# Kernel optimization log

Hardware: AMD Instinct MI355X
Metric: run time of the kernel (lower is better)

Reference implementation:

```python
import jax, jax.numpy as jnp
import numpy as np

N, E, IN, HID, H, L, G = 20000, 320000, 128, 64, 4, 3, 128

def setup_inputs() -> dict:
    key = jax.random.key(0)
    ks = jax.random.split(key, 14)
    x = jax.random.normal(ks[0], (N, IN), dtype=jnp.float32)
    edge_index = jax.random.randint(ks[1], (2, E), 0, N, dtype=jnp.int64)
    batch = jnp.sort(jax.random.randint(ks[2], (N,), 0, G, dtype=jnp.int64))
    s_in = 1.0 / np.sqrt(IN)
    s_h = 1.0 / np.sqrt(HID)
    lin_W = jax.random.normal(ks[3], (IN, HID), jnp.float32) * s_in
    lin_b = jax.random.normal(ks[4], (HID,), jnp.float32) * 0.02
    Wq = jax.random.normal(ks[5], (L, HID, H * HID), jnp.float32) * s_h
    bq = jax.random.normal(ks[6], (L, H * HID), jnp.float32) * 0.02
    Wk = jax.random.normal(ks[7], (L, HID, H * HID), jnp.float32) * s_h
    bk = jax.random.normal(ks[8], (L, H * HID), jnp.float32) * 0.02
    Wv = jax.random.normal(ks[9], (L, HID, H * HID), jnp.float32) * s_h
    bv = jax.random.normal(ks[10], (L, H * HID), jnp.float32) * 0.02
    Ws = jax.random.normal(ks[11], (L, HID, HID), jnp.float32) * s_h
    bs = jax.random.normal(ks[12], (L, HID), jnp.float32) * 0.02
    return {"x": x, "edge_index": edge_index, "batch": batch,
            "lin_W": lin_W, "lin_b": lin_b, "Wq": Wq, "bq": bq,
            "Wk": Wk, "bk": bk, "Wv": Wv, "bv": bv, "Ws": Ws, "bs": bs}

def _transformer_conv(h, src, dst, Wq, bq, Wk, bk, Wv, bv, Ws, bs):
    # PyG TransformerConv(hid, hid, heads=H, concat=False), beta=False, root_weight=True
    n = h.shape[0]
    C = HID  # per-head dim
    q = (h @ Wq + bq).reshape(n, H, C)
    k = (h @ Wk + bk).reshape(n, H, C)
    v = (h @ Wv + bv).reshape(n, H, C)
    # per-edge attention logits: q_i . k_j / sqrt(C), i=dst (target), j=src
    alpha = jnp.einsum('ehc,ehc->eh', q[dst], k[src]) * (1.0 / np.sqrt(C))  # [E,H]
    # segment softmax over edges grouped by target node
    amax = jax.ops.segment_max(alpha, dst, num_segments=n)  # [N,H]
    amax = jnp.where(jnp.isfinite(amax), amax, 0.0)
    ex = jnp.exp(alpha - amax[dst])
    denom = jax.ops.segment_sum(ex, dst, num_segments=n)
    a = ex / jnp.maximum(denom[dst], 1e-16)  # [E,H]
    msg = a[:, :, None] * v[src]  # [E,H,C]
    agg = jax.ops.segment_sum(msg.reshape(-1, H * C), dst, num_segments=n)
    out = agg.reshape(n, H, C).mean(axis=1)  # concat=False -> head mean
    return out + h @ Ws + bs  # root/skip connection

def reference(x, edge_index, batch, lin_W, lin_b, Wq, bq, Wk, bk, Wv, bv, Ws, bs):
    src, dst = edge_index[0], edge_index[1]
    h = x @ lin_W + lin_b  # [N, HID]; dropout inactive in eval
    for l in range(L):
        h = jax.nn.relu(_transformer_conv(h, src, dst, Wq[l], bq[l], Wk[l], bk[l],
                                          Wv[l], bv[l], Ws[l], bs[l]))
    # global_add_pool: sum node features per graph
    return jax.ops.segment_sum(h, batch, num_segments=G)  # [G, HID]
```

## Files before the change

### kernel.cpp

```cpp
#include <hip/hip_runtime.h>
#include <math.h>

#define N_NODES 20000
#define N_EDGES 320000
#define DIM_IN 128
#define HID 64
#define HEADS 4
#define LAYERS 3
#define GRAPHS 128
#define QSS 320

typedef unsigned short ushort;
typedef ushort ushort8 __attribute__((ext_vector_type(8)));
typedef short short8 __attribute__((ext_vector_type(8)));
typedef float f32x4 __attribute__((ext_vector_type(4)));

__device__ __forceinline__ float bf2f(ushort u) {
    return __uint_as_float(((unsigned int)u) << 16);
}
__device__ __forceinline__ ushort f2bf(float f) {
    unsigned int b = __float_as_uint(f);
    return (ushort)((b + 0x7FFFu + ((b >> 16) & 1u)) >> 16);
}


__global__ void hist_kernel(const int* __restrict__ dst, int* __restrict__ counts, int n) {
    int e = blockIdx.x * 256 + threadIdx.x;
    if (e < n) atomicAdd(&counts[dst[e]], 1);
}

__global__ __launch_bounds__(256) void blocksum_kernel(const int* __restrict__ counts,
                                                       int* __restrict__ bsum, int n) {
    int i = blockIdx.x * 256 + threadIdx.x;
    int v = (i < n) ? counts[i] : 0;
    int lane = threadIdx.x & 63, wave = threadIdx.x >> 6;
#pragma unroll
    for (int off = 32; off >= 1; off >>= 1) v += __shfl_xor(v, off);
    __shared__ int ws[4];
    if (lane == 0) ws[wave] = v;
    __syncthreads();
    if (threadIdx.x == 0) bsum[blockIdx.x] = ws[0] + ws[1] + ws[2] + ws[3];
}

__global__ __launch_bounds__(128) void scanb_kernel(const int* __restrict__ bsum,
                                                    int* __restrict__ bexcl, int nb) {
    int tid = threadIdx.x;
    int v = (tid < nb) ? bsum[tid] : 0;
    int lane = tid & 63, wave = tid >> 6;
    int s = v;
#pragma unroll
    for (int off = 1; off < 64; off <<= 1) {
        int t = __shfl_up(s, off);
        if (lane >= off) s += t;
    }
    __shared__ int w0sum;
    if (tid == 63) w0sum = s;
    __syncthreads();
    int excl = s - v + (wave ? w0sum : 0);
    if (tid < nb) bexcl[tid] = excl;
}

__global__ __launch_bounds__(256) void expand_kernel(const int* __restrict__ counts,
                                                     const int* __restrict__ bexcl,
                                                     int* __restrict__ offs,
                                                     int* __restrict__ cursor, int n) {
    int i = blockIdx.x * 256 + threadIdx.x;
    int v = (i < n) ? counts[i] : 0;
    int lane = threadIdx.x & 63, wave = threadIdx.x >> 6;
    int s = v;
#pragma unroll
    for (int off = 1; off < 64; off <<= 1) {
        int t = __shfl_up(s, off);
        if (lane >= off) s += t;
    }
    __shared__ int wsum[4];
    if (lane == 63) wsum[wave] = s;
    __syncthreads();
    int add = bexcl[blockIdx.x];
    for (int w = 0; w < wave; ++w) add += wsum[w];
    int excl = add + s - v;
    if (i < n) { offs[i] = excl; cursor[i] = excl; }
    if (i == 0) offs[n] = N_EDGES;
}

__global__ void scatter_kernel(const int* __restrict__ src, const int* __restrict__ dst,
                               int* __restrict__ cursor, int* __restrict__ csr, int n) {
    int e = blockIdx.x * 256 + threadIdx.x;
    if (e < n) {
        int d = dst[e];
        int pos = atomicAdd(&cursor[d], 1);
        csr[pos] = src[e];
    }
}


__global__ __launch_bounds__(256) void lin_kernel(const float* __restrict__ x,
                                                  const float* __restrict__ W,
                                                  const float* __restrict__ b,
                                                  float* __restrict__ h0) {
    __shared__ float xt[32][DIM_IN];
    int tx = threadIdx.x;
    int row0 = blockIdx.x * 32;
    for (int idx = tx; idx < 32 * DIM_IN; idx += 256) {
        int r = idx / DIM_IN, c = idx % DIM_IN;
        xt[r][c] = x[(size_t)(row0 + r) * DIM_IN + c];
    }
    __syncthreads();
    int col = tx & 63;
    int sub = tx >> 6;
    float acc[8];
#pragma unroll
    for (int r = 0; r < 8; ++r) acc[r] = 0.f;
    for (int k = 0; k < DIM_IN; k += 4) {
        float w0 = W[k * HID + col];
        float w1 = W[(k + 1) * HID + col];
        float w2 = W[(k + 2) * HID + col];
        float w3 = W[(k + 3) * HID + col];
#pragma unroll
        for (int r = 0; r < 8; ++r) {
            const float4 hv = *(const float4*)&xt[r * 4 + sub][k];
            acc[r] += hv.x * w0 + hv.y * w1 + hv.z * w2 + hv.w * w3;
        }
    }
    float bias = b[col];
#pragma unroll
    for (int r = 0; r < 8; ++r) {
        int row = row0 + r * 4 + sub;
        h0[(size_t)row * HID + col] = acc[r] + bias;
    }
}


__global__ __launch_bounds__(256) void wcvt_kernel(const float* __restrict__ Wq, const float* __restrict__ bq,
                                                   const float* __restrict__ Wk, const float* __restrict__ bk,
                                                   const float* __restrict__ Wv, const float* __restrict__ bv,
                                                   const float* __restrict__ Ws, const float* __restrict__ bs,
                                                   ushort* __restrict__ Wt, float* __restrict__ bias_cat) {
    int idx = blockIdx.x * 256 + threadIdx.x;
    if (idx < 832 * 64) {
        int j = idx >> 6, k = idx & 63;
        float w;
        if (j < 256)      w = Wq[(size_t)k * 256 + j];
        else if (j < 512) w = Wk[(size_t)k * 256 + (j - 256)];
        else if (j < 768) w = Wv[(size_t)k * 256 + (j - 512)];
        else              w = Ws[(size_t)k * 64 + (j - 768)];
        Wt[idx] = f2bf(w);
    }
    if (idx < 832) {
        float b;
        if (idx < 256)      b = bq[idx];
        else if (idx < 512) b = bk[idx - 256];
        else if (idx < 768) b = bv[idx - 512];
        else                b = bs[idx - 768];
        bias_cat[idx] = b;
    }
}


__global__ __launch_bounds__(512) void proj_kernel(const float* __restrict__ h,
                                                   const ushort* __restrict__ Wt,
                                                   const float* __restrict__ bias_cat,
                                                   float* __restrict__ qs,
                                                   ushort* __restrict__ kvpack) {
    int tid = threadIdx.x;
    int w = tid >> 6, l = tid & 63;
    int r0 = blockIdx.x * 32 + (w & 1) * 16;
    int c0 = (w >> 1) * 208;
    int row = r0 + (l & 15);
    int koff = (l >> 4) * 8;

    short8 a[2];
#pragma unroll
    for (int m = 0; m < 2; ++m) {
        const float* hp = h + (size_t)row * HID + m * 32 + koff;
        float4 f0 = *(const float4*)hp;
        float4 f1 = *(const float4*)(hp + 4);
        ushort8 u;
        u[0] = f2bf(f0.x); u[1] = f2bf(f0.y); u[2] = f2bf(f0.z); u[3] = f2bf(f0.w);
        u[4] = f2bf(f1.x); u[5] = f2bf(f1.y); u[6] = f2bf(f1.z); u[7] = f2bf(f1.w);
        a[m] = __builtin_bit_cast(short8, u);
    }

    f32x4 acc[13];
#pragma unroll
    for (int t = 0; t < 13; ++t) acc[t] = (f32x4){0.f, 0.f, 0.f, 0.f};

    const ushort* wb = Wt + ((size_t)(c0 + (l & 15))) * HID + koff;
#pragma unroll
    for (int t = 0; t < 13; ++t) {
        short8 b0 = *(const short8*)(wb + (size_t)t * 16 * HID);
        short8 b1 = *(const short8*)(wb + (size_t)t * 16 * HID + 32);
        acc[t] = __builtin_amdgcn_mfma_f32_16x16x32_bf16(a[0], b0, acc[t], 0, 0, 0);
        acc[t] = __builtin_amdgcn_mfma_f32_16x16x32_bf16(a[1], b1, acc[t], 0, 0, 0);
    }

    int colbase = c0 + (l & 15);
    int rbase = r0 + ((l >> 4) << 2);
#pragma unroll
    for (int t = 0; t < 13; ++t) {
        int j = colbase + t * 16;
        float bias = bias_cat[j];
        if (j < 256) {
#pragma unroll
            for (int i = 0; i < 4; ++i)
                qs[(size_t)(rbase + i) * QSS + j] = acc[t][i] + bias;
        } else if (j < 768) {
            int ck = j - 256;
            int isv = ck >> 8;
            int ch = ck & 255;
            int hh2 = ch >> 6, c = ch & 63;
            int pos = (hh2 * 16 + (c >> 2)) * 8 + isv * 4 + (c & 3);
#pragma unroll
            for (int i = 0; i < 4; ++i)
                kvpack[(size_t)(rbase + i) * 512 + pos] = f2bf(acc[t][i] + bias);
        } else {
#pragma unroll
            for (int i = 0; i < 4; ++i)
                qs[(size_t)(rbase + i) * QSS + 256 + (j - 768)] = acc[t][i] + bias;
        }
    }
}


__global__ __launch_bounds__(256) void edge_kernel(const float* __restrict__ qs,
                                                   const ushort8* __restrict__ kvp,
                                                   const int* __restrict__ offs,
                                                   const int* __restrict__ csr,
                                                   float* __restrict__ hout) {
    int wave = threadIdx.x >> 6;
    int lane = threadIdx.x & 63;
    int node = blockIdx.x * 4 + wave;
    if (node >= N_NODES) return;
    int hh = lane >> 4;
    int cb = (lane & 15) * 4;

    const float* nb = qs + (size_t)node * QSS;
    float4 q = *(const float4*)(nb + hh * 64 + cb);

    float m = -INFINITY, l = 0.f;
    float4 acc = make_float4(0.f, 0.f, 0.f, 0.f);

    int e0 = offs[node], e1 = offs[node + 1];
    int cnt = e1 - e0;

    ushort8 cur = (ushort8)(0);
    ushort8 nxt = (ushort8)(0);
    if (cnt > 0) cur = kvp[(size_t)csr[e0] * 64 + lane];
    if (cnt > 1) nxt = kvp[(size_t)csr[e0 + 1] * 64 + lane];

    for (int i = 0; i < cnt; ++i) {
        ushort8 u = cur;
        cur = nxt;
        if (i + 2 < cnt) nxt = kvp[(size_t)csr[e0 + i + 2] * 64 + lane];

        float p = q.x * bf2f(u[0]) + q.y * bf2f(u[1]) + q.z * bf2f(u[2]) + q.w * bf2f(u[3]);
        p += __shfl_xor(p, 1);
        p += __shfl_xor(p, 2);
        p += __shfl_xor(p, 4);
        p += __shfl_xor(p, 8);
        float alpha = p * 0.125f;
        float nm = fmaxf(m, alpha);
        float sc = __expf(m - nm);
        float pe = __expf(alpha - nm);
        l = l * sc + pe;
        acc.x = acc.x * sc + pe * bf2f(u[4]);
        acc.y = acc.y * sc + pe * bf2f(u[5]);
        acc.z = acc.z * sc + pe * bf2f(u[6]);
        acc.w = acc.w * sc + pe * bf2f(u[7]);
        m = nm;
    }

    float inv = (l > 0.f) ? (1.f / l) : 0.f;
    float4 r;
    r.x = acc.x * inv;
    r.y = acc.y * inv;
    r.z = acc.z * inv;
    r.w = acc.w * inv;
    r.x += __shfl_xor(r.x, 16); r.x += __shfl_xor(r.x, 32);
    r.y += __shfl_xor(r.y, 16); r.y += __shfl_xor(r.y, 32);
    r.z += __shfl_xor(r.z, 16); r.z += __shfl_xor(r.z, 32);
    r.w += __shfl_xor(r.w, 16); r.w += __shfl_xor(r.w, 32);

    if (hh == 0) {
        float4 s = *(const float4*)(nb + 256 + cb);
        float4 o;
        o.x = fmaxf(r.x * 0.25f + s.x, 0.f);
        o.y = fmaxf(r.y * 0.25f + s.y, 0.f);
        o.z = fmaxf(r.z * 0.25f + s.z, 0.f);
        o.w = fmaxf(r.w * 0.25f + s.w, 0.f);
        *(float4*)(hout + (size_t)node * HID + cb) = o;
    }
}


__global__ __launch_bounds__(256) void pool_kernel(const float* __restrict__ h,
                                                   const int* __restrict__ batch,
                                                   float* __restrict__ out) {
    int g = blockIdx.x;
    int lo = 0, hi = N_NODES;
    while (lo < hi) { int mid = (lo + hi) >> 1; if (batch[mid] < g) lo = mid + 1; else hi = mid; }
    int start = lo;
    hi = N_NODES;
    while (lo < hi) { int mid = (lo + hi) >> 1; if (batch[mid] < g + 1) lo = mid + 1; else hi = mid; }
    int end = lo;
    int c = threadIdx.x & 63;
    int sub = threadIdx.x >> 6;
    float acc = 0.f;
    for (int i = start + sub; i < end; i += 4) acc += h[(size_t)i * HID + c];
    __shared__ float lds[4][64];
    lds[sub][c] = acc;
    __syncthreads();
    if (sub == 0) out[g * HID + c] = lds[0][c] + lds[1][c] + lds[2][c] + lds[3][c];
}


extern "C" void kernel_launch(void* const* d_in, const int* in_sizes, int n_in,
                              void* d_out, int out_size, void* d_ws, size_t ws_size,
                              hipStream_t stream) {
    const float* x    = (const float*)d_in[0];
    const int*   edge = (const int*)d_in[1];
    const int*   batch= (const int*)d_in[2];
    const float* linW = (const float*)d_in[3];
    const float* linb = (const float*)d_in[4];
    const float* Wq   = (const float*)d_in[5];
    const float* bq   = (const float*)d_in[6];
    const float* Wk   = (const float*)d_in[7];
    const float* bk   = (const float*)d_in[8];
    const float* Wv   = (const float*)d_in[9];
    const float* bv   = (const float*)d_in[10];
    const float* Ws   = (const float*)d_in[11];
    const float* bs   = (const float*)d_in[12];
    float* out = (float*)d_out;

    const int* src = edge;
    const int* dst = edge + N_EDGES;

    float* h0  = (float*)d_ws;
    float* h1  = h0 + (size_t)N_NODES * HID;
    float* qs  = h1 + (size_t)N_NODES * HID;
    ushort* kvpack = (ushort*)(qs + (size_t)N_NODES * QSS);
    int* counts = (int*)(kvpack + (size_t)N_NODES * 512);
    int* offs   = counts + N_NODES;
    int* cursor = offs + N_NODES + 1;
    int* csr    = cursor + N_NODES;
    int* bsum   = csr + N_EDGES;
    int* bexcl  = bsum + 128;
    ushort* Wt  = (ushort*)(bexcl + 128);
    float* bias_cat = (float*)(Wt + 832 * 64);

    const int NB = (N_NODES + 255) / 256;

    hipMemsetAsync(counts, 0, N_NODES * sizeof(int), stream);
    hist_kernel<<<(N_EDGES + 255) / 256, 256, 0, stream>>>(dst, counts, N_EDGES);
    blocksum_kernel<<<NB, 256, 0, stream>>>(counts, bsum, N_NODES);
    scanb_kernel<<<1, 128, 0, stream>>>(bsum, bexcl, NB);
    expand_kernel<<<NB, 256, 0, stream>>>(counts, bexcl, offs, cursor, N_NODES);
    scatter_kernel<<<(N_EDGES + 255) / 256, 256, 0, stream>>>(src, dst, cursor, csr, N_EDGES);

    lin_kernel<<<N_NODES / 32, 256, 0, stream>>>(x, linW, linb, h0);

    float* hc = h0;
    float* hn = h1;
    for (int l = 0; l < LAYERS; ++l) {
        wcvt_kernel<<<(832 * 64 + 255) / 256, 256, 0, stream>>>(
            Wq + (size_t)l * HID * 256, bq + (size_t)l * 256,
            Wk + (size_t)l * HID * 256, bk + (size_t)l * 256,
            Wv + (size_t)l * HID * 256, bv + (size_t)l * 256,
            Ws + (size_t)l * HID * 64,  bs + (size_t)l * 64,
            Wt, bias_cat);
        proj_kernel<<<N_NODES / 32, 512, 0, stream>>>(hc, Wt, bias_cat, qs, kvpack);
        edge_kernel<<<N_NODES / 4, 256, 0, stream>>>(qs, (const ushort8*)kvpack, offs, csr, hn);
        float* t = hc; hc = hn; hn = t;
    }

    pool_kernel<<<GRAPHS, 256, 0, stream>>>(hc, batch, out);
}
```

Before: 404.3 us.

## Batch weight conversion, MFMA input linear, and 8-deep edge prefetch with lazy rescale

Merges the three per-layer weight conversion launches, plus a bf16 transpose of the input linear weight, into one kernel. The K/V interleave permutation moves from proj_kernel's store into the weight layout, so stores become contiguous. The input linear layer switches from scalar FP32 to bf16 MFMA. The edge kernel now prefetches 8 neighbor rows at a time and rescales the online softmax only when some lane's max increases. Together these cut launches and hide gather latency, at the cost of more registers and bf16 rounding of the input x.

```diff
diff --git a/kernel.cpp b/kernel.cpp
--- a/kernel.cpp
+++ b/kernel.cpp
@@ -94,65 +94,111 @@
 }
 
 
+__global__ __launch_bounds__(256) void wcvt_all_kernel(
+        const float* __restrict__ Wq, const float* __restrict__ bq,
+        const float* __restrict__ Wk, const float* __restrict__ bk,
+        const float* __restrict__ Wv, const float* __restrict__ bv,
+        const float* __restrict__ Ws, const float* __restrict__ bs,
+        const float* __restrict__ linW,
+        ushort* __restrict__ Wt3, float* __restrict__ bias3,
+        ushort* __restrict__ Wlt) {
+    const int PER = 832 * 64;
+    int idx = blockIdx.x * 256 + threadIdx.x;
+    if (idx < 3 * PER) {
+        int l = idx / PER;
+        int r = idx - l * PER;
+        int j = r >> 6, k = r & 63;
+        const float* Wq_l = Wq + (size_t)l * HID * 256;
+        const float* Wk_l = Wk + (size_t)l * HID * 256;
+        const float* Wv_l = Wv + (size_t)l * HID * 256;
+        const float* Ws_l = Ws + (size_t)l * HID * 64;
+        float w;
+        if (j < 256) {
+            w = Wq_l[(size_t)k * 256 + j];
+        } else if (j < 768) {
+            int pout = j - 256;
+            int isv = (pout >> 2) & 1;
+            int low2 = pout & 3;
+            int g = pout >> 3;
+            int srccol = (g >> 4) * 64 + (g & 15) * 4 + low2;
+            w = isv ? Wv_l[(size_t)k * 256 + srccol] : Wk_l[(size_t)k * 256 + srccol];
+        } else {
+            w = Ws_l[(size_t)k * 64 + (j - 768)];
+        }
+        Wt3[idx] = f2bf(w);
+    } else {
+        int idx2 = idx - 3 * PER;
+        if (idx2 < 64 * DIM_IN) {
+            int col = idx2 >> 7, k = idx2 & 127;
+            Wlt[idx2] = f2bf(linW[(size_t)k * HID + col]);
+        }
+    }
+    if (idx < 3 * 832) {
+        int l = idx / 832, j = idx - l * 832;
+        float b;
+        if (j < 256) {
+            b = bq[l * 256 + j];
+        } else if (j < 768) {
+            int pout = j - 256;
+            int isv = (pout >> 2) & 1;
+            int low2 = pout & 3;
+            int g = pout >> 3;
+            int srccol = (g >> 4) * 64 + (g & 15) * 4 + low2;
+            b = isv ? bv[l * 256 + srccol] : bk[l * 256 + srccol];
+        } else {
+            b = bs[l * 64 + (j - 768)];
+        }
+        bias3[idx] = b;
+    }
+}
+
+
 __global__ __launch_bounds__(256) void lin_kernel(const float* __restrict__ x,
-                                                  const float* __restrict__ W,
-                                                  const float* __restrict__ b,
+                                                  const ushort* __restrict__ Wlt,
+                                                  const float* __restrict__ lb,
                                                   float* __restrict__ h0) {
-    __shared__ float xt[32][DIM_IN];
-    int tx = threadIdx.x;
-    int row0 = blockIdx.x * 32;
-    for (int idx = tx; idx < 32 * DIM_IN; idx += 256) {
-        int r = idx / DIM_IN, c = idx % DIM_IN;
-        xt[r][c] = x[(size_t)(row0 + r) * DIM_IN + c];
-    }
-    __syncthreads();
-    int col = tx & 63;
-    int sub = tx >> 6;
-    float acc[8];
-#pragma unroll
-    for (int r = 0; r < 8; ++r) acc[r] = 0.f;
-    for (int k = 0; k < DIM_IN; k += 4) {
-        float w0 = W[k * HID + col];
-        float w1 = W[(k + 1) * HID + col];
-        float w2 = W[(k + 2) * HID + col];
-        float w3 = W[(k + 3) * HID + col];
-#pragma unroll
-        for (int r = 0; r < 8; ++r) {
-            const float4 hv = *(const float4*)&xt[r * 4 + sub][k];
-            acc[r] += hv.x * w0 + hv.y * w1 + hv.z * w2 + hv.w * w3;
-        }
-    }
-    float bias = b[col];
-#pragma unroll
-    for (int r = 0; r < 8; ++r) {
-        int row = row0 + r * 4 + sub;
-        h0[(size_t)row * HID + col] = acc[r] + bias;
-    }
-}
-
-
-__global__ __launch_bounds__(256) void wcvt_kernel(const float* __restrict__ Wq, const float* __restrict__ bq,
-                                                   const float* __restrict__ Wk, const float* __restrict__ bk,
-                                                   const float* __restrict__ Wv, const float* __restrict__ bv,
-                                                   const float* __restrict__ Ws, const float* __restrict__ bs,
-                                                   ushort* __restrict__ Wt, float* __restrict__ bias_cat) {
-    int idx = blockIdx.x * 256 + threadIdx.x;
-    if (idx < 832 * 64) {
-        int j = idx >> 6, k = idx & 63;
-        float w;
-        if (j < 256)      w = Wq[(size_t)k * 256 + j];
-        else if (j < 512) w = Wk[(size_t)k * 256 + (j - 256)];
-        else if (j < 768) w = Wv[(size_t)k * 256 + (j - 512)];
-        else              w = Ws[(size_t)k * 64 + (j - 768)];
-        Wt[idx] = f2bf(w);
-    }
-    if (idx < 832) {
-        float b;
-        if (idx < 256)      b = bq[idx];
-        else if (idx < 512) b = bk[idx - 256];
-        else if (idx < 768) b = bv[idx - 512];
-        else                b = bs[idx - 768];
-        bias_cat[idx] = b;
+    int tid = threadIdx.x;
+    int w = tid >> 6, l = tid & 63;
+    int r0 = blockIdx.x * 64 + w * 16;
+    int row = r0 + (l & 15);
+    int rowc = (row < N_NODES) ? row : (N_NODES - 1);
+
+    short8 a[4];
+#pragma unroll
+    for (int kc = 0; kc < 4; ++kc) {
+        const float* xp = x + (size_t)rowc * DIM_IN + kc * 32 + (l >> 4) * 8;
+        float4 f0 = *(const float4*)xp;
+        float4 f1 = *(const float4*)(xp + 4);
+        ushort8 u;
+        u[0] = f2bf(f0.x); u[1] = f2bf(f0.y); u[2] = f2bf(f0.z); u[3] = f2bf(f0.w);
+        u[4] = f2bf(f1.x); u[5] = f2bf(f1.y); u[6] = f2bf(f1.z); u[7] = f2bf(f1.w);
+        a[kc] = __builtin_bit_cast(short8, u);
+    }
+
+    f32x4 acc[4];
+#pragma unroll
+    for (int t = 0; t < 4; ++t) acc[t] = (f32x4){0.f, 0.f, 0.f, 0.f};
+
+    const ushort* wb = Wlt + (size_t)(l & 15) * DIM_IN + (l >> 4) * 8;
+#pragma unroll
+    for (int t = 0; t < 4; ++t) {
+#pragma unroll
+        for (int kc = 0; kc < 4; ++kc) {
+            short8 b = *(const short8*)(wb + (size_t)t * 16 * DIM_IN + kc * 32);
+            acc[t] = __builtin_amdgcn_mfma_f32_16x16x32_bf16(a[kc], b, acc[t], 0, 0, 0);
+        }
+    }
+
+    int rbase = r0 + ((l >> 4) << 2);
+#pragma unroll
+    for (int t = 0; t < 4; ++t) {
+        int col = t * 16 + (l & 15);
+        float bias = lb[col];
+#pragma unroll
+        for (int i = 0; i < 4; ++i) {
+            int rr = rbase + i;
+            if (rr < N_NODES) h0[(size_t)rr * HID + col] = acc[t][i] + bias;
+        }
     }
 }
 
@@ -205,14 +251,10 @@
             for (int i = 0; i < 4; ++i)
                 qs[(size_t)(rbase + i) * QSS + j] = acc[t][i] + bias;
         } else if (j < 768) {
-            int ck = j - 256;
-            int isv = ck >> 8;
-            int ch = ck & 255;
-            int hh2 = ch >> 6, c = ch & 63;
-            int pos = (hh2 * 16 + (c >> 2)) * 8 + isv * 4 + (c & 3);
+            int pout = j - 256;
 #pragma unroll
             for (int i = 0; i < 4; ++i)
-                kvpack[(size_t)(rbase + i) * 512 + pos] = f2bf(acc[t][i] + bias);
+                kvpack[(size_t)(rbase + i) * 512 + pout] = f2bf(acc[t][i] + bias);
         } else {
 #pragma unroll
             for (int i = 0; i < 4; ++i)
@@ -221,6 +263,29 @@
     }
 }
 
+
+#define LD1(DST, EI) { int ee = (EI) < e1 ? (EI) : (e1 - 1); DST = kvp[(size_t)csr[ee] * 64 + lane]; }
+
+#define PROC(U, EI) do { \
+    float p = q.x * bf2f(U[0]) + q.y * bf2f(U[1]) + q.z * bf2f(U[2]) + q.w * bf2f(U[3]); \
+    p += __shfl_xor(p, 1); \
+    p += __shfl_xor(p, 2); \
+    p += __shfl_xor(p, 4); \
+    p += __shfl_xor(p, 8); \
+    float alpha = ((EI) < e1) ? p * 0.125f : -INFINITY; \
+    if (__any(alpha > m)) { \
+        float nm = fmaxf(m, alpha); \
+        float sc = __expf(m - nm); \
+        l *= sc; acc.x *= sc; acc.y *= sc; acc.z *= sc; acc.w *= sc; \
+        m = nm; \
+    } \
+    float pe = __expf(alpha - m); \
+    l += pe; \
+    acc.x += pe * bf2f(U[4]); \
+    acc.y += pe * bf2f(U[5]); \
+    acc.z += pe * bf2f(U[6]); \
+    acc.w += pe * bf2f(U[7]); \
+} while (0)
 
 __global__ __launch_bounds__(256) void edge_kernel(const float* __restrict__ qs,
                                                    const ushort8* __restrict__ kvp,
@@ -243,31 +308,24 @@
     int e0 = offs[node], e1 = offs[node + 1];
     int cnt = e1 - e0;
 
-    ushort8 cur = (ushort8)(0);
-    ushort8 nxt = (ushort8)(0);
-    if (cnt > 0) cur = kvp[(size_t)csr[e0] * 64 + lane];
-    if (cnt > 1) nxt = kvp[(size_t)csr[e0 + 1] * 64 + lane];
-
-    for (int i = 0; i < cnt; ++i) {
-        ushort8 u = cur;
-        cur = nxt;
-        if (i + 2 < cnt) nxt = kvp[(size_t)csr[e0 + i + 2] * 64 + lane];
-
-        float p = q.x * bf2f(u[0]) + q.y * bf2f(u[1]) + q.z * bf2f(u[2]) + q.w * bf2f(u[3]);
-        p += __shfl_xor(p, 1);
-        p += __shfl_xor(p, 2);
-        p += __shfl_xor(p, 4);
-        p += __shfl_xor(p, 8);
-        float alpha = p * 0.125f;
-        float nm = fmaxf(m, alpha);
-        float sc = __expf(m - nm);
-        float pe = __expf(alpha - nm);
-        l = l * sc + pe;
-        acc.x = acc.x * sc + pe * bf2f(u[4]);
-        acc.y = acc.y * sc + pe * bf2f(u[5]);
-        acc.z = acc.z * sc + pe * bf2f(u[6]);
-        acc.w = acc.w * sc + pe * bf2f(u[7]);
-        m = nm;
+    if (cnt > 0) {
+        ushort8 A0, A1, A2, A3, A4, A5, A6, A7;
+        LD1(A0, e0 + 0); LD1(A1, e0 + 1); LD1(A2, e0 + 2); LD1(A3, e0 + 3);
+        LD1(A4, e0 + 4); LD1(A5, e0 + 5); LD1(A6, e0 + 6); LD1(A7, e0 + 7);
+        for (int base = e0; base < e1; base += 8) {
+            ushort8 B0, B1, B2, B3, B4, B5, B6, B7;
+            bool more = (base + 8) < e1;
+            if (more) {
+                LD1(B0, base + 8);  LD1(B1, base + 9);  LD1(B2, base + 10); LD1(B3, base + 11);
+                LD1(B4, base + 12); LD1(B5, base + 13); LD1(B6, base + 14); LD1(B7, base + 15);
+            }
+            PROC(A0, base + 0); PROC(A1, base + 1); PROC(A2, base + 2); PROC(A3, base + 3);
+            PROC(A4, base + 4); PROC(A5, base + 5); PROC(A6, base + 6); PROC(A7, base + 7);
+            if (more) {
+                A0 = B0; A1 = B1; A2 = B2; A3 = B3;
+                A4 = B4; A5 = B5; A6 = B6; A7 = B7;
+            }
+        }
     }
 
     float inv = (l > 0.f) ? (1.f / l) : 0.f;
@@ -345,8 +403,9 @@
     int* csr    = cursor + N_NODES;
     int* bsum   = csr + N_EDGES;
     int* bexcl  = bsum + 128;
-    ushort* Wt  = (ushort*)(bexcl + 128);
-    float* bias_cat = (float*)(Wt + 832 * 64);
+    ushort* Wt3 = (ushort*)(bexcl + 128);
+    float* bias3 = (float*)(Wt3 + 3 * 832 * 64);
+    ushort* Wlt = (ushort*)(bias3 + 3 * 832);
 
     const int NB = (N_NODES + 255) / 256;
 
@@ -357,18 +416,16 @@
     expand_kernel<<<NB, 256, 0, stream>>>(counts, bexcl, offs, cursor, N_NODES);
     scatter_kernel<<<(N_EDGES + 255) / 256, 256, 0, stream>>>(src, dst, cursor, csr, N_EDGES);
 
-    lin_kernel<<<N_NODES / 32, 256, 0, stream>>>(x, linW, linb, h0);
+    wcvt_all_kernel<<<(3 * 832 * 64 + 64 * DIM_IN + 255) / 256, 256, 0, stream>>>(
+        Wq, bq, Wk, bk, Wv, bv, Ws, bs, linW, Wt3, bias3, Wlt);
+
+    lin_kernel<<<(N_NODES + 63) / 64, 256, 0, stream>>>(x, Wlt, linb, h0);
 
     float* hc = h0;
     float* hn = h1;
     for (int l = 0; l < LAYERS; ++l) {
-        wcvt_kernel<<<(832 * 64 + 255) / 256, 256, 0, stream>>>(
-            Wq + (size_t)l * HID * 256, bq + (size_t)l * 256,
-            Wk + (size_t)l * HID * 256, bk + (size_t)l * 256,
-            Wv + (size_t)l * HID * 256, bv + (size_t)l * 256,
-            Ws + (size_t)l * HID * 64,  bs + (size_t)l * 64,
-            Wt, bias_cat);
-        proj_kernel<<<N_NODES / 32, 512, 0, stream>>>(hc, Wt, bias_cat, qs, kvpack);
+        proj_kernel<<<N_NODES / 32, 512, 0, stream>>>(hc,
+            Wt3 + (size_t)l * 832 * 64, bias3 + (size_t)l * 832, qs, kvpack);
         edge_kernel<<<N_NODES / 4, 256, 0, stream>>>(qs, (const ushort8*)kvpack, offs, csr, hn);
         float* t = hc; hc = hn; hn = t;
     }
```

After: 396.5 us. No clear change (-1.9%).
